# Performance work log

Hardware: AMD Instinct MI355X
Metric: run time of the kernel (lower is better)

## Reference

```python
import jax, jax.numpy as jnp
import numpy as np

NUM_HEADS = 16


def sinusoidal_pe(N, C, dtype=jnp.float32):
    # matches the numpy construction in get_positional_encoding
    pos = jnp.arange(N, dtype=dtype)[:, None]                  # [N,1]
    dims = jnp.arange(C)                                        # [C]
    rates = 1.0 / jnp.power(jnp.asarray(10000.0, dtype), (2 * (dims // 2)).astype(dtype) / C)
    ang = pos * rates                                           # [N,C]
    pe = jnp.where(dims % 2 == 0, jnp.sin(ang), jnp.cos(ang))
    return pe.astype(dtype)


def setup_inputs() -> dict:
    key = jax.random.key(0)
    k1, k2, k3 = jax.random.split(key, 3)
    B, N, C = 4, 2048, 1024
    inputs = jax.random.normal(k1, (B, N, C), dtype=jnp.float32)
    mask_mat = jax.random.uniform(k2, (B, N), dtype=jnp.float32)
    # Glorot-uniform qkv kernel [C, 3C]
    limit = float(np.sqrt(6.0 / (C + 3 * C)))
    W_qkv = jax.random.uniform(k3, (C, 3 * C), dtype=jnp.float32, minval=-limit, maxval=limit)
    return {"inputs": inputs, "mask_mat": mask_mat, "W_qkv": W_qkv}


def reference(inputs, mask_mat, W_qkv):
    B, N, C = inputs.shape
    H = NUM_HEADS
    hd = C // H
    scale = hd ** (-0.5)

    # additive mask: -(m outer m), broadcast over heads
    neg_mask = -(mask_mat[:, :, None] * mask_mat[:, None, :])   # [B,N,N]

    x = inputs + sinusoidal_pe(N, C, inputs.dtype)              # APE
    qkv = jnp.einsum('bnc,cd->bnd', x, W_qkv)                   # [B,N,3C]
    qkv = qkv.reshape(B, N, 3, H, hd).transpose(2, 0, 3, 1, 4)  # [3,B,H,N,hd]
    q, k, v = qkv[0], qkv[1], qkv[2]

    attn = jnp.einsum('bhnd,bhmd->bhnm', q, k) * scale          # [B,H,N,N]
    attn = attn + neg_mask[:, None, :, :]
    attn = jax.nn.softmax(attn, axis=-1)
    out = jnp.einsum('bhnm,bhmd->bhnd', attn, v)                # [B,H,N,hd]
    return out.transpose(0, 2, 1, 3).reshape(B, N, C)
```

## Files before the change

### kernel.cpp

```cpp
#include <hip/hip_runtime.h>
#include <hip/hip_bf16.h>

typedef unsigned short u16;
typedef __bf16 bf16x8 __attribute__((ext_vector_type(8)));
typedef float floatx4 __attribute__((ext_vector_type(4)));

#define B_ 4
#define N_ 2048
#define C_ 1024
#define H_ 16
#define HD_ 64

__device__ __forceinline__ float b2f(u16 u) {
    union { float f; unsigned int i; } v; v.i = ((unsigned int)u) << 16; return v.f;
}
__device__ __forceinline__ u16 f2b(float f) {
    union { float f; unsigned int i; } v; v.f = f;
    unsigned int i = v.i;
    unsigned int r = i + 0x7FFFu + ((i >> 16) & 1u);
    return (u16)(r >> 16);
}
__device__ __forceinline__ unsigned int pk2(float a, float b) {
    __hip_bfloat162 t = __float22bfloat162_rn(float2{a, b});
    unsigned int u; __builtin_memcpy(&u, &t, 4); return u;
}
__device__ __forceinline__ void async16(const u16* g, u16* l) {
    __builtin_amdgcn_global_load_lds((const __attribute__((address_space(1))) unsigned int*)g,
                                     (__attribute__((address_space(3))) unsigned int*)l,
                                     16, 0, 0);
}

__global__ __launch_bounds__(256) void pe_add_kernel(const float* __restrict__ in,
                                                     u16* __restrict__ x) {
    int idx = blockIdx.x * 256 + threadIdx.x;
    int cp  = idx & 511;
    int row = idx >> 9;
    int n   = row & (N_ - 1);
    float r = exp2f(-13.287712379549449f * ((float)cp * (1.0f / 512.0f)));
    float ang = (float)n * r;
    float s, c;
    sincosf(ang, &s, &c);
    float2 pr = ((const float2*)in)[idx];
    unsigned int o = ((unsigned int)f2b(pr.y + c) << 16) | (unsigned int)f2b(pr.x + s);
    ((unsigned int*)x)[idx] = o;
}

__global__ __launch_bounds__(256) void wt_kernel(const float* __restrict__ W,
                                                 u16* __restrict__ Wt) {
    __shared__ u16 tile[32][33];
    int bx = blockIdx.x;
    int by = blockIdx.y;
    int tx = threadIdx.x & 31;
    int ty = threadIdx.x >> 5;
    for (int i = 0; i < 32; i += 8)
        tile[ty + i][tx] = f2b(W[(size_t)(by * 32 + ty + i) * 3072 + bx * 32 + tx]);
    __syncthreads();
    for (int i = 0; i < 32; i += 8)
        Wt[(size_t)(bx * 32 + ty + i) * 1024 + by * 32 + tx] = tile[tx][ty + i];
}

__global__ __launch_bounds__(256) void qkv_gemm_kernel(const u16* __restrict__ X,
                                                       const u16* __restrict__ Wt,
                                                       u16* __restrict__ q,
                                                       u16* __restrict__ k,
                                                       u16* __restrict__ vt) {
    __shared__ u16 As[128 * 64];
    __shared__ u16 Bs[128 * 64];
    int tid  = threadIdx.x;
    int wave = tid >> 6, lane = tid & 63, l15 = lane & 15, quad = lane >> 4;
    int m0 = blockIdx.x * 128;
    int n0 = blockIdx.y * 128;
    int wm = (wave & 1) * 64;
    int wn = (wave >> 1) * 64;

    floatx4 acc[4][4];
    for (int i = 0; i < 4; i++)
        for (int j = 0; j < 4; j++)
            acc[i][j] = floatx4{0.f, 0.f, 0.f, 0.f};

    int rowOff = wave * 32 + (lane >> 3);
    int colSw  = ((lane & 7) ^ (lane >> 3)) * 8;
    const u16* gA = X  + (size_t)(m0 + rowOff) * 1024 + colSw;
    const u16* gB = Wt + (size_t)(n0 + rowOff) * 1024 + colSw;
    u16* lA = As + wave * 2048;
    u16* lB = Bs + wave * 2048;

    int swl = l15 & 7;
    int aB0 = (wm + l15) * 64 + ((quad ^ swl) * 8);
    int aB1 = (wm + l15) * 64 + (((4 + quad) ^ swl) * 8);
    int bB0 = (wn + l15) * 64 + ((quad ^ swl) * 8);
    int bB1 = (wn + l15) * 64 + (((4 + quad) ^ swl) * 8);

    for (int k0 = 0; k0 < 1024; k0 += 64) {
        __syncthreads();
        async16(gA + k0,             lA);
        async16(gA + k0 +  8 * 1024, lA + 512);
        async16(gA + k0 + 16 * 1024, lA + 1024);
        async16(gA + k0 + 24 * 1024, lA + 1536);
        async16(gB + k0,             lB);
        async16(gB + k0 +  8 * 1024, lB + 512);
        async16(gB + k0 + 16 * 1024, lB + 1024);
        async16(gB + k0 + 24 * 1024, lB + 1536);
        __syncthreads();

        bf16x8 af[4][2], bf[4][2];
        for (int i = 0; i < 4; i++) {
            af[i][0] = *(const bf16x8*)(As + aB0 + i * 16 * 64);
            af[i][1] = *(const bf16x8*)(As + aB1 + i * 16 * 64);
        }
        for (int j = 0; j < 4; j++) {
            bf[j][0] = *(const bf16x8*)(Bs + bB0 + j * 16 * 64);
            bf[j][1] = *(const bf16x8*)(Bs + bB1 + j * 16 * 64);
        }
        for (int i = 0; i < 4; i++)
            for (int j = 0; j < 4; j++) {
                acc[i][j] = __builtin_amdgcn_mfma_f32_16x16x32_bf16(af[i][0], bf[j][0], acc[i][j], 0, 0, 0);
                acc[i][j] = __builtin_amdgcn_mfma_f32_16x16x32_bf16(af[i][1], bf[j][1], acc[i][j], 0, 0, 0);
            }
    }

    const float QSC = 0.125f * 1.44269504f;
    for (int i = 0; i < 4; i++) {
        int gm   = m0 + wm + i * 16 + quad * 4;
        int b    = gm >> 11;
        int nloc = gm & 2047;
        for (int j = 0; j < 4; j++) {
            int gn    = n0 + wn + j * 16 + l15;
            int which = gn >> 10;
            int cc    = gn & 1023;
            int h     = cc >> 6;
            int d     = cc & 63;
            size_t bh = (size_t)(b * 16 + h);
            if (which == 2) {
                ushort4 w4;
                w4.x = f2b(acc[i][j][0]);
                w4.y = f2b(acc[i][j][1]);
                w4.z = f2b(acc[i][j][2]);
                w4.w = f2b(acc[i][j][3]);
                *(ushort4*)(vt + (bh * 64 + d) * 2048 + nloc) = w4;
            } else {
                u16* dst = (which == 0) ? q : k;
                float sc = (which == 0) ? QSC : 1.0f;
                for (int r = 0; r < 4; r++)
                    dst[(bh * 2048 + nloc + r) * 64 + d] = f2b(acc[i][j][r] * sc);
            }
        }
    }
}

__global__ __launch_bounds__(256, 3) void attn_kernel(const u16* __restrict__ q,
                                                      const u16* __restrict__ k,
                                                      const u16* __restrict__ vt,
                                                      const float* __restrict__ mask,
                                                      float* __restrict__ out) {
    __shared__ u16 Ks[4][32 * 64];
    __shared__ u16 Vs[4][64 * 32];
    __shared__ u16 Ps[4][32 * 40];
    __shared__ __align__(16) float Ms[2048];

    int tid  = threadIdx.x;
    int wave = tid >> 6, lane = tid & 63, l15 = lane & 15, quad = lane >> 4;
    int bid = blockIdx.x;
    int bh = bid & 63, qb = bid >> 6;
    int b = bh >> 4, h = bh & 15;
    size_t base = (size_t)bh * (N_ * 64);
    int q0 = qb * 128 + wave * 32;
    const float* mkb = mask + b * N_;

    {
        float4 m0 = *(const float4*)(mkb + tid * 8);
        float4 m1 = *(const float4*)(mkb + tid * 8 + 4);
        *(float4*)(Ms + tid * 8)     = m0;
        *(float4*)(Ms + tid * 8 + 4) = m1;
    }

    bf16x8 qf[2][2];
#pragma unroll
    for (int s = 0; s < 2; s++)
#pragma unroll
        for (int dc = 0; dc < 2; dc++)
            qf[s][dc] = *(const bf16x8*)(q + base + (size_t)(q0 + s * 16 + l15) * 64 + dc * 32 + quad * 8);

    const float L2E = 1.44269504f;
    float nmq[2];
    nmq[0] = -L2E * mkb[q0 + l15];
    nmq[1] = -L2E * mkb[q0 + 16 + l15];

    bf16x8 onef;
#pragma unroll
    for (int i = 0; i < 8; i++) onef[i] = (__bf16)1.0f;

    floatx4 acc[2][4];
    floatx4 accl[2];
#pragma unroll
    for (int s = 0; s < 2; s++) {
        accl[s] = floatx4{0.f, 0.f, 0.f, 0.f};
#pragma unroll
        for (int dt = 0; dt < 4; dt++)
            acc[s][dt] = floatx4{0.f, 0.f, 0.f, 0.f};
    }

    int krow = wave * 8  + (lane >> 3);
    int kcol = ((lane & 7) ^ (lane >> 3)) * 8;
    int vrow = wave * 16 + (lane >> 2);
    int vcol = ((lane & 3) ^ ((lane >> 2) & 3)) * 8;
    const u16* gK = k  + base + (size_t)krow * 64 + kcol;
    const u16* gV = vt + ((size_t)bh * 64 + vrow) * 2048 + vcol;
    int wof = wave * 512;

    int a0 = ((quad    ) ^ (l15 & 7)) * 8;
    int a1 = ((4 + quad) ^ (l15 & 7)) * 8;
    int av = ( quad      ^ (l15 & 3)) * 8;

    u16* Pw = Ps[wave];

    auto TILE = [&](int kt, const u16* Kb, const u16* Vb, u16* Kn, u16* Vn) {
        asm volatile("s_waitcnt vmcnt(2)" ::: "memory");
        __builtin_amdgcn_s_barrier();
        __builtin_amdgcn_sched_barrier(0);
        int nkt = kt + 64; if (nkt > N_ - 32) nkt = N_ - 32;
        async16(gK + (size_t)nkt * 64, Kn);
        async16(gV + nkt,              Vn);
        float4 mkv0 = *(const float4*)(Ms + kt + quad * 4);
        float4 mkv1 = *(const float4*)(Ms + kt + 16 + quad * 4);
#pragma unroll
        for (int t = 0; t < 2; t++) {
            bf16x8 kf0 = *(const bf16x8*)(Kb + (t * 16 + l15) * 64 + a0);
            bf16x8 kf1 = *(const bf16x8*)(Kb + (t * 16 + l15) * 64 + a1);
            float4 mk = t ? mkv1 : mkv0;
#pragma unroll
            for (int s = 0; s < 2; s++) {
                floatx4 sa;
                sa[0] = nmq[s] * mk.x;
                sa[1] = nmq[s] * mk.y;
                sa[2] = nmq[s] * mk.z;
                sa[3] = nmq[s] * mk.w;
                __builtin_amdgcn_s_setprio(1);
                sa = __builtin_amdgcn_mfma_f32_16x16x32_bf16(kf0, qf[s][0], sa, 0, 0, 0);
                sa = __builtin_amdgcn_mfma_f32_16x16x32_bf16(kf1, qf[s][1], sa, 0, 0, 0);
                __builtin_amdgcn_s_setprio(0);
                float p0 = exp2f(sa[0]);
                float p1 = exp2f(sa[1]);
                float p2 = exp2f(sa[2]);
                float p3 = exp2f(sa[3]);
                uint2 w; w.x = pk2(p0, p1); w.y = pk2(p2, p3);
                *(uint2*)(Pw + (s * 16 + l15) * 40 + t * 16 + quad * 4) = w;
            }
        }
        bf16x8 pf0 = *(const bf16x8*)(Pw + l15 * 40 + quad * 8);
        bf16x8 pf1 = *(const bf16x8*)(Pw + (16 + l15) * 40 + quad * 8);
        __builtin_amdgcn_s_setprio(1);
        accl[0] = __builtin_amdgcn_mfma_f32_16x16x32_bf16(pf0, onef, accl[0], 0, 0, 0);
        accl[1] = __builtin_amdgcn_mfma_f32_16x16x32_bf16(pf1, onef, accl[1], 0, 0, 0);
        __builtin_amdgcn_s_setprio(0);
#pragma unroll
        for (int dt = 0; dt < 4; dt++) {
            bf16x8 vf = *(const bf16x8*)(Vb + (dt * 16 + l15) * 32 + av);
            __builtin_amdgcn_s_setprio(1);
            acc[0][dt] = __builtin_amdgcn_mfma_f32_16x16x32_bf16(pf0, vf, acc[0][dt], 0, 0, 0);
            acc[1][dt] = __builtin_amdgcn_mfma_f32_16x16x32_bf16(pf1, vf, acc[1][dt], 0, 0, 0);
            __builtin_amdgcn_s_setprio(0);
        }
    };

    async16(gK,           Ks[0] + wof);
    async16(gV,           Vs[0] + wof);
    async16(gK + 32 * 64, Ks[1] + wof);
    async16(gV + 32,      Vs[1] + wof);
    __syncthreads();

    for (int m = 0; m < 16; ++m) {
        int kt = m * 128;
        TILE(kt,      Ks[0], Vs[0], Ks[2] + wof, Vs[2] + wof);
        TILE(kt + 32, Ks[1], Vs[1], Ks[3] + wof, Vs[3] + wof);
        TILE(kt + 64, Ks[2], Vs[2], Ks[0] + wof, Vs[0] + wof);
        TILE(kt + 96, Ks[3], Vs[3], Ks[1] + wof, Vs[1] + wof);
    }

#pragma unroll
    for (int s = 0; s < 2; s++) {
#pragma unroll
        for (int r = 0; r < 4; r++) {
            float ir = 1.0f / accl[s][r];
            int qrow = q0 + s * 16 + quad * 4 + r;
            float* orow = out + ((size_t)(b * N_ + qrow)) * C_ + h * 64;
#pragma unroll
            for (int dt = 0; dt < 4; dt++)
                orow[dt * 16 + l15] = acc[s][dt][r] * ir;
        }
    }
}

extern "C" void kernel_launch(void* const* d_in, const int* in_sizes, int n_in,
                              void* d_out, int out_size, void* d_ws, size_t ws_size,
                              hipStream_t stream) {
    const float* inp  = (const float*)d_in[0];
    const float* mask = (const float*)d_in[1];
    const float* W    = (const float*)d_in[2];
    float* out = (float*)d_out;

    char* ws = (char*)d_ws;
    u16* x  = (u16*)ws;
    u16* Wt = (u16*)(ws + 16777216);
    u16* q  = (u16*)(ws + 23068672);
    u16* k  = q + 8388608;
    u16* vt = k + 8388608;

    pe_add_kernel<<<16384, 256, 0, stream>>>(inp, x);
    wt_kernel<<<dim3(96, 32), 256, 0, stream>>>(W, Wt);
    qkv_gemm_kernel<<<dim3(64, 24), 256, 0, stream>>>(x, Wt, q, k, vt);
    attn_kernel<<<1024, 256, 0, stream>>>(q, k, vt, mask, out);
}
```

Before: 280.6 us.

## Shrink attention LDS footprint with triple-buffering and streamed mask for higher occupancy

```diff
diff --git a/kernel.cpp b/kernel.cpp
--- a/kernel.cpp
+++ b/kernel.cpp
@@ -25,6 +25,11 @@
     unsigned int u; __builtin_memcpy(&u, &t, 4); return u;
 }
 __device__ __forceinline__ void async16(const u16* g, u16* l) {
+    __builtin_amdgcn_global_load_lds((const __attribute__((address_space(1))) unsigned int*)g,
+                                     (__attribute__((address_space(3))) unsigned int*)l,
+                                     16, 0, 0);
+}
+__device__ __forceinline__ void async16p(const void* g, void* l) {
     __builtin_amdgcn_global_load_lds((const __attribute__((address_space(1))) unsigned int*)g,
                                      (__attribute__((address_space(3))) unsigned int*)l,
                                      16, 0, 0);
@@ -148,15 +153,15 @@
     }
 }
 
-__global__ __launch_bounds__(256, 3) void attn_kernel(const u16* __restrict__ q,
+__global__ __launch_bounds__(256, 4) void attn_kernel(const u16* __restrict__ q,
                                                       const u16* __restrict__ k,
                                                       const u16* __restrict__ vt,
                                                       const float* __restrict__ mask,
                                                       float* __restrict__ out) {
-    __shared__ u16 Ks[4][32 * 64];
-    __shared__ u16 Vs[4][64 * 32];
+    __shared__ u16 Ks[3][32 * 64];
+    __shared__ u16 Vs[3][64 * 32];
     __shared__ u16 Ps[4][32 * 40];
-    __shared__ __align__(16) float Ms[2048];
+    __shared__ __align__(16) float Msr[3][256];
 
     int tid  = threadIdx.x;
     int wave = tid >> 6, lane = tid & 63, l15 = lane & 15, quad = lane >> 4;
@@ -167,13 +172,6 @@
     int q0 = qb * 128 + wave * 32;
     const float* mkb = mask + b * N_;
 
-    {
-        float4 m0 = *(const float4*)(mkb + tid * 8);
-        float4 m1 = *(const float4*)(mkb + tid * 8 + 4);
-        *(float4*)(Ms + tid * 8)     = m0;
-        *(float4*)(Ms + tid * 8 + 4) = m1;
-    }
-
     bf16x8 qf[2][2];
 #pragma unroll
     for (int s = 0; s < 2; s++)
@@ -206,6 +204,7 @@
     int vcol = ((lane & 3) ^ ((lane >> 2) & 3)) * 8;
     const u16* gK = k  + base + (size_t)krow * 64 + kcol;
     const u16* gV = vt + ((size_t)bh * 64 + vrow) * 2048 + vcol;
+    const float* gM = mkb + (lane & 7) * 4;
     int wof = wave * 512;
 
     int a0 = ((quad    ) ^ (l15 & 7)) * 8;
@@ -214,15 +213,17 @@
 
     u16* Pw = Ps[wave];
 
-    auto TILE = [&](int kt, const u16* Kb, const u16* Vb, u16* Kn, u16* Vn) {
-        asm volatile("s_waitcnt vmcnt(2)" ::: "memory");
+    auto TILE = [&](int kt, const u16* Kb, const u16* Vb, const float* Mb,
+                    u16* Kn, u16* Vn, float* Mn) {
+        asm volatile("s_waitcnt vmcnt(3)" ::: "memory");
         __builtin_amdgcn_s_barrier();
         __builtin_amdgcn_sched_barrier(0);
         int nkt = kt + 64; if (nkt > N_ - 32) nkt = N_ - 32;
         async16(gK + (size_t)nkt * 64, Kn);
         async16(gV + nkt,              Vn);
-        float4 mkv0 = *(const float4*)(Ms + kt + quad * 4);
-        float4 mkv1 = *(const float4*)(Ms + kt + 16 + quad * 4);
+        async16p(gM + nkt,             Mn);
+        float4 mkv0 = *(const float4*)(Mb + quad * 4);
+        float4 mkv1 = *(const float4*)(Mb + 16 + quad * 4);
 #pragma unroll
         for (int t = 0; t < 2; t++) {
             bf16x8 kf0 = *(const bf16x8*)(Kb + (t * 16 + l15) * 64 + a0);
@@ -263,19 +264,22 @@
         }
     };
 
-    async16(gK,           Ks[0] + wof);
-    async16(gV,           Vs[0] + wof);
-    async16(gK + 32 * 64, Ks[1] + wof);
-    async16(gV + 32,      Vs[1] + wof);
+    asm volatile("s_waitcnt vmcnt(0)" ::: "memory");
+    async16(gK,            Ks[0] + wof);
+    async16(gV,            Vs[0] + wof);
+    async16p(gM,           Msr[0]);
+    async16(gK + 32 * 64,  Ks[1] + wof);
+    async16(gV + 32,       Vs[1] + wof);
+    async16p(gM + 32,      Msr[1]);
     __syncthreads();
 
-    for (int m = 0; m < 16; ++m) {
-        int kt = m * 128;
-        TILE(kt,      Ks[0], Vs[0], Ks[2] + wof, Vs[2] + wof);
-        TILE(kt + 32, Ks[1], Vs[1], Ks[3] + wof, Vs[3] + wof);
-        TILE(kt + 64, Ks[2], Vs[2], Ks[0] + wof, Vs[0] + wof);
-        TILE(kt + 96, Ks[3], Vs[3], Ks[1] + wof, Vs[1] + wof);
-    }
+    for (int m = 0; m < 21; ++m) {
+        int kt = m * 96;
+        TILE(kt,      Ks[0], Vs[0], Msr[0], Ks[2] + wof, Vs[2] + wof, Msr[2]);
+        TILE(kt + 32, Ks[1], Vs[1], Msr[1], Ks[0] + wof, Vs[0] + wof, Msr[0]);
+        TILE(kt + 64, Ks[2], Vs[2], Msr[2], Ks[1] + wof, Vs[1] + wof, Msr[1]);
+    }
+    TILE(2016, Ks[0], Vs[0], Msr[0], Ks[2] + wof, Vs[2] + wof, Msr[2]);
 
 #pragma unroll
     for (int s = 0; s < 2; s++) {
```

After: 270.0 us. 1.04x faster.
